# Performance work log

Measured on AMD Instinct MI355X. Metric: run time of the kernel, lower is better.

The kernel has to match this reference:

```python
import jax, jax.numpy as jnp
import numpy as np

EMBED_DIM = 512
NUM_HEADS = 8
HEAD_DIM = EMBED_DIM // NUM_HEADS
REL_MAX = 16
NUM_POS_IDS = 2 * REL_MAX + 1 + 1  # 34 (directed + padding id)
PADDING_IDX = 0
B, S = 2, 2048


def setup_inputs() -> dict:
    key = jax.random.key(0)
    ks = jax.random.split(key, 9)
    Q = jax.random.normal(ks[0], (B, S, EMBED_DIM), dtype=jnp.float32)
    K = jax.random.normal(ks[1], (B, S, EMBED_DIM), dtype=jnp.float32)
    V = jax.random.normal(ks[2], (B, S, EMBED_DIM), dtype=jnp.float32)
    rel_pos_ids = jax.random.randint(ks[3], (B, S, S), 0, NUM_POS_IDS, dtype=jnp.int64) if jax.config.jax_enable_x64 else jax.random.randint(ks[3], (B, S, S), 0, NUM_POS_IDS, dtype=jnp.int32)
    scale = 0.02
    Wq = jax.random.normal(ks[4], (EMBED_DIM, EMBED_DIM), dtype=jnp.float32) * scale
    Wk = jax.random.normal(ks[5], (EMBED_DIM, EMBED_DIM), dtype=jnp.float32) * scale
    Wv = jax.random.normal(ks[6], (EMBED_DIM, EMBED_DIM), dtype=jnp.float32) * scale
    Wo = jax.random.normal(ks[7], (EMBED_DIM, EMBED_DIM), dtype=jnp.float32) * scale
    rel_emb = jax.random.normal(ks[8], (NUM_POS_IDS, EMBED_DIM), dtype=jnp.float32) * scale
    rel_emb = rel_emb.at[PADDING_IDX].set(0.0)  # nn.Embedding padding_idx row is zero
    return {"Q": Q, "K": K, "V": V, "rel_pos_ids": rel_pos_ids,
            "Wq": Wq, "Wk": Wk, "Wv": Wv, "Wo": Wo, "rel_emb": rel_emb}


def _proj(x, W):
    # Linear (no bias) then strided head split: view(B, S, head_dim, H) -> (B, H, S, head_dim)
    b, s, _ = x.shape
    y = x @ W.T
    return y.reshape(b, s, HEAD_DIM, NUM_HEADS).transpose(0, 3, 1, 2)


def _forward(Q, K, V, rel_pos_ids, Wq, Wk, Wv, Wo, rel_emb):
    b, sq, _ = Q.shape
    Qp = _proj(Q, Wq)  # (B, H, Sq, hd)
    Kp = _proj(K, Wk)  # (B, H, Sk, hd)
    Vp = _proj(V, Wv)  # (B, H, Sk, hd)

    # rel_embeds split per head with the same strided layout: (P, hd, H) -> (H, P, hd)
    R = rel_emb.reshape(NUM_POS_IDS, HEAD_DIM, NUM_HEADS).transpose(2, 0, 1)
    # Q_rel: (B, H, Sq, P)
    Q_rel = jnp.einsum('bhsd,hpd->bhsp', Qp, R)
    # gather per-pair relative bias: (B, H, Sq, Sk)
    rel_shift = jnp.take_along_axis(Q_rel, rel_pos_ids[:, None, :, :], axis=3)
    mask = (rel_pos_ids == PADDING_IDX)[:, None, :, :]
    rel_shift = jnp.where(mask, -jnp.inf, rel_shift)

    energy = (jnp.einsum('bhqd,bhkd->bhqk', Qp, Kp) + rel_shift) / jnp.sqrt(jnp.float32(HEAD_DIM))
    attn = jax.nn.softmax(energy, axis=-1)
    out = jnp.einsum('bhqk,bhkd->bhqd', attn, Vp)  # (B, H, Sq, hd)
    # inverse of strided split: (B, Sq, hd, H) -> flatten last two
    out = out.transpose(0, 2, 3, 1).reshape(b, sq, EMBED_DIM)
    return out @ Wo.T


def reference(Q, K, V, rel_pos_ids, Wq, Wk, Wv, Wo, rel_emb):
    return _forward(Q, K, V, rel_pos_ids, Wq, Wk, Wv, Wo, rel_emb)
```

## Files before the change

### kernel.cpp

```cpp
#include <hip/hip_runtime.h>
#include <cstdint>
#include <cstddef>

#define SEQ   2048
#define BBAT  2
#define EMBED 512
#define NH    8
#define HD    64
#define NPOS  34

typedef __bf16 bf16;
typedef __bf16 bf16x8 __attribute__((ext_vector_type(8)));
typedef float  f32x4  __attribute__((ext_vector_type(4)));
typedef int    int32x4 __attribute__((ext_vector_type(4)));

#define ESCALE 0.1803368801111204f

__device__ __forceinline__ f32x4 mfma16(bf16x8 a, bf16x8 b, f32x4 c){
  return __builtin_amdgcn_mfma_f32_16x16x32_bf16(a, b, c, 0, 0, 0);
}

__global__ __launch_bounds__(256) void k_prep(
    const float* __restrict__ Q, const float* __restrict__ K, const float* __restrict__ V,
    const float* __restrict__ Wq, const float* __restrict__ Wk,
    const float* __restrict__ Wv, const float* __restrict__ Wo,
    const float* __restrict__ RE,
    bf16* __restrict__ Qb, bf16* __restrict__ Kb, bf16* __restrict__ Vb,
    bf16* __restrict__ Wall, bf16* __restrict__ Rb)
{
  const int NCONV = 3*524288;
  const int NW = 196608, NO = 262144;
  int i = blockIdx.x*256 + threadIdx.x;
  if (i < NCONV){
    int tsel = i >> 19, j = i & 524287;
    const float* s = tsel==0 ? Q : (tsel==1 ? K : V);
    bf16* d       = tsel==0 ? Qb : (tsel==1 ? Kb : Vb);
    float4 v = ((const float4*)s)[j];
    union { bf16 e[4]; ushort4 u; } pk;
    pk.e[0]=(bf16)v.x; pk.e[1]=(bf16)v.y; pk.e[2]=(bf16)v.z; pk.e[3]=(bf16)v.w;
    ((ushort4*)d)[j] = pk.u;
  } else {
    int j = i - NCONV;
    if (j < NW){
      int w  = j >> 16;
      int r  = j & 65535;
      int np = r >> 7, c4 = (r & 127) << 2;
      const float* W = (w==0) ? Wq : ((w==1) ? Wk : Wv);
      int src = ((np & 63) << 3) + (np >> 6);
      float4 v = *(const float4*)(W + (size_t)src*512 + c4);
      union { bf16 e[4]; ushort4 u; } pk;
      pk.e[0]=(bf16)v.x; pk.e[1]=(bf16)v.y; pk.e[2]=(bf16)v.z; pk.e[3]=(bf16)v.w;
      *(ushort4*)(Wall + (size_t)w*262144 + (size_t)np*512 + c4) = pk.u;
    } else if (j < NW + NO){
      int jj = j - NW;
      int n = jj >> 9, kp = jj & 511;
      int src = ((kp & 63) << 3) + (kp >> 6);
      Wall[(size_t)3*262144 + (size_t)n*512 + kp] = (bf16)Wo[(size_t)n*512 + src];
    } else {
      int jj = j - NW - NO;
      if (jj < 8*48*64){
        int h  = jj / (48*64);
        int r2 = jj - h*(48*64);
        int p  = r2 >> 6, dd = r2 & 63;
        float v = (p < NPOS) ? RE[(size_t)p*512 + dd*8 + h] : 0.f;
        Rb[jj] = (bf16)v;
      }
    }
  }
}

__global__ __launch_bounds__(256,2) void k_gemm_proj(
    const bf16* __restrict__ Qb, const bf16* __restrict__ Kb, const bf16* __restrict__ Vb,
    const bf16* __restrict__ W,  bf16* __restrict__ Qp, bf16* __restrict__ Kp, bf16* __restrict__ Vt)
{
  const bf16* A  = blockIdx.z==0 ? Qb : (blockIdx.z==1 ? Kb : Vb);
  const bf16* Bw = W + (size_t)blockIdx.z*262144;

  __shared__ __align__(16) bf16 As[128][72];
  __shared__ __align__(16) bf16 Bs[64][72];
  const int t = threadIdx.x;
  const int w = t >> 6, lane = t & 63, l15 = lane & 15, quad = lane >> 4;
  const int wm = (w & 1) * 64, wn = (w >> 1) * 32;
  const int m0 = blockIdx.y * 128, n0 = blockIdx.x * 64;

  f32x4 acc[4][2];
  #pragma unroll
  for (int mt=0; mt<4; ++mt)
    #pragma unroll
    for (int nt=0; nt<2; ++nt) acc[mt][nt] = (f32x4){0.f,0.f,0.f,0.f};

  for (int kt = 0; kt < 512; kt += 64){
    #pragma unroll
    for (int i = 0; i < 4; ++i){
      int lin = t + 256*i;
      int r = lin >> 3, c8 = (lin & 7) << 3;
      *(uint4*)&As[r][c8] = *(const uint4*)(A + (size_t)(m0 + r)*512 + kt + c8);
    }
    #pragma unroll
    for (int i = 0; i < 2; ++i){
      int lin = t + 256*i;
      int r = lin >> 3, c8 = (lin & 7) << 3;
      *(uint4*)&Bs[r][c8] = *(const uint4*)(Bw + (size_t)(n0 + r)*512 + kt + c8);
    }
    __syncthreads();
    #pragma unroll
    for (int ks = 0; ks < 2; ++ks){
      bf16x8 am[4], bn[2];
      #pragma unroll
      for (int x=0;x<4;++x) am[x] = *(const bf16x8*)&As[wm + x*16 + l15][ks*32 + quad*8];
      #pragma unroll
      for (int y=0;y<2;++y) bn[y] = *(const bf16x8*)&Bs[wn + y*16 + l15][ks*32 + quad*8];
      #pragma unroll
      for (int mt=0;mt<4;++mt)
        #pragma unroll
        for (int nt=0;nt<2;++nt)
          acc[mt][nt] = mfma16(am[mt], bn[nt], acc[mt][nt]);
    }
    __syncthreads();
  }

  if (blockIdx.z != 2){
    bf16* C = blockIdx.z==0 ? Qp : Kp;
    const float scl = (blockIdx.z==0) ? ESCALE : 1.0f;
    #pragma unroll
    for (int mt=0;mt<4;++mt)
      #pragma unroll
      for (int r=0;r<4;++r){
        int m = m0 + wm + mt*16 + quad*4 + r;
        #pragma unroll
        for (int nt=0;nt<2;++nt)
          C[(size_t)m*512 + n0 + wn + nt*16 + l15] = (bf16)(acc[mt][nt][r] * scl);
      }
  } else {
    bf16 (*VT)[136] = (bf16(*)[136])As;
    #pragma unroll
    for (int mt=0;mt<4;++mt)
      #pragma unroll
      for (int r=0;r<4;++r){
        int m = wm + mt*16 + quad*4 + r;
        #pragma unroll
        for (int nt=0;nt<2;++nt)
          VT[wn + nt*16 + l15][m] = (bf16)acc[mt][nt][r];
      }
    __syncthreads();
    const int h = blockIdx.x, b = m0 >> 11, s0 = m0 & 2047;
    const int n = t >> 2, c0 = (t & 3) * 32;
    bf16* dst = Vt + ((size_t)((b*NH + h)*HD + n))*SEQ + s0 + c0;
    #pragma unroll
    for (int i = 0; i < 4; ++i)
      *(uint4*)(dst + i*8) = *(const uint4*)&VT[n][c0 + i*8];
  }
}

__global__ __launch_bounds__(256,2) void k_gemm_out(
    const bf16* __restrict__ A, const bf16* __restrict__ Bw, float* __restrict__ C)
{
  __shared__ __align__(16) bf16 As[64][72];
  __shared__ __align__(16) bf16 Bs[64][72];
  const int t = threadIdx.x;
  const int w = t >> 6, lane = t & 63, l15 = lane & 15, quad = lane >> 4;
  const int wm = (w & 1) * 32, wn = (w >> 1) * 32;
  const int m0 = blockIdx.y * 64, n0 = blockIdx.x * 64;

  f32x4 acc[2][2];
  #pragma unroll
  for (int mt=0; mt<2; ++mt)
    #pragma unroll
    for (int nt=0; nt<2; ++nt) acc[mt][nt] = (f32x4){0.f,0.f,0.f,0.f};

  for (int kt = 0; kt < 512; kt += 64){
    #pragma unroll
    for (int i = 0; i < 2; ++i){
      int lin = t + 256*i;
      int r = lin >> 3, c8 = (lin & 7) << 3;
      *(uint4*)&As[r][c8] = *(const uint4*)(A  + (size_t)(m0 + r)*512 + kt + c8);
      *(uint4*)&Bs[r][c8] = *(const uint4*)(Bw + (size_t)(n0 + r)*512 + kt + c8);
    }
    __syncthreads();
    #pragma unroll
    for (int ks = 0; ks < 2; ++ks){
      bf16x8 am[2], bn[2];
      #pragma unroll
      for (int x=0;x<2;++x) am[x] = *(const bf16x8*)&As[wm + x*16 + l15][ks*32 + quad*8];
      #pragma unroll
      for (int y=0;y<2;++y) bn[y] = *(const bf16x8*)&Bs[wn + y*16 + l15][ks*32 + quad*8];
      #pragma unroll
      for (int mt=0;mt<2;++mt)
        #pragma unroll
        for (int nt=0;nt<2;++nt)
          acc[mt][nt] = mfma16(am[mt], bn[nt], acc[mt][nt]);
    }
    __syncthreads();
  }
  #pragma unroll
  for (int mt=0;mt<2;++mt)
    #pragma unroll
    for (int r=0;r<4;++r){
      int m = m0 + wm + mt*16 + quad*4 + r;
      #pragma unroll
      for (int nt=0;nt<2;++nt)
        C[(size_t)m*512 + n0 + wn + nt*16 + l15] = acc[mt][nt][r];
    }
}

__global__ __launch_bounds__(256,2) void k_attn(
    const bf16* __restrict__ Qp, const bf16* __restrict__ Kp,
    const bf16* __restrict__ Vt, const bf16* __restrict__ Rb,
    const int* __restrict__ ids, bf16* __restrict__ Out)
{
  __shared__ __align__(16) bf16 Ks[128][72];
  __shared__ __align__(16) bf16 Vs[64][136];
  __shared__ __align__(16) bf16 Ps[64][136];
  __shared__ float lut[64][35];
  __shared__ float lsum_s[128];

  const int t = threadIdx.x;
  const int b = blockIdx.z, h = blockIdx.y;
  const int q0 = blockIdx.x * 64;
  const int w = t >> 6, lane = t & 63, l15 = lane & 15, quad = lane >> 4;
  const int qh = w & 1, kh = w >> 1;

  const size_t idb = (size_t)b*SEQ*SEQ;

  int32x4 nid[2][4];
  #pragma unroll
  for (int mt=0; mt<2; ++mt)
    #pragma unroll
    for (int nt=0; nt<4; ++nt)
      nid[mt][nt] = *(const int32x4*)(ids + idb
          + (size_t)(q0 + qh*32 + mt*16 + l15)*SEQ
          + kh*64 + nt*16 + quad*4);

  {
    const bf16* qbrow = Qp + (size_t)(b*SEQ + q0 + w*16 + l15)*EMBED + h*HD;
    bf16x8 ab0 = *(const bf16x8*)(qbrow + quad*8);
    bf16x8 ab1 = *(const bf16x8*)(qbrow + 32 + quad*8);
    const bf16* rh = Rb + h*3072;
    #pragma unroll
    for (int nt = 0; nt < 3; ++nt){
      bf16x8 r0 = *(const bf16x8*)(rh + (nt*16 + l15)*64 + quad*8);
      bf16x8 r1 = *(const bf16x8*)(rh + (nt*16 + l15)*64 + 32 + quad*8);
      f32x4 c = (f32x4){0.f,0.f,0.f,0.f};
      c = mfma16(ab0, r0, c);
      c = mfma16(ab1, r1, c);
      int p = nt*16 + l15;
      if (p < NPOS){
        #pragma unroll
        for (int r = 0; r < 4; ++r)
          lut[w*16 + quad*4 + r][p] = (p == 0) ? -1e30f : c[r];
      }
    }
  }

  bf16x8 bq[2][2];
  #pragma unroll
  for (int mt = 0; mt < 2; ++mt){
    const bf16* qrow = Qp + (size_t)(b*SEQ + q0 + qh*32 + mt*16 + l15)*EMBED + h*HD;
    bq[mt][0] = *(const bf16x8*)(qrow + quad*8);
    bq[mt][1] = *(const bf16x8*)(qrow + 32 + quad*8);
  }

  const bf16* kbase = Kp + (size_t)b*SEQ*EMBED + h*HD;
  const bf16* vbase = Vt + (size_t)(b*NH + h)*HD*SEQ;

  f32x4 acc[2][2];
  #pragma unroll
  for (int mt=0;mt<2;++mt)
    #pragma unroll
    for (int nt=0;nt<2;++nt) acc[mt][nt] = (f32x4){0.f,0.f,0.f,0.f};
  float lsum[2] = {0.f, 0.f};

  for (int kt = 0; kt < 16; ++kt){
    const int k0 = kt * 128;
    #pragma unroll
    for (int i = 0; i < 4; ++i){
      int lin = t + 256*i;
      int r = lin >> 3, c8 = (lin & 7) << 3;
      *(uint4*)&Ks[r][c8] = *(const uint4*)(kbase + (size_t)(k0 + r)*EMBED + c8);
    }
    #pragma unroll
    for (int i = 0; i < 4; ++i){
      int lin = t + 256*i;
      int d = lin >> 4, c8 = (lin & 15) << 3;
      *(uint4*)&Vs[d][c8] = *(const uint4*)(vbase + (size_t)d*SEQ + k0 + c8);
    }
    __syncthreads();

    float wv[2][4][4];
    #pragma unroll
    for (int mt = 0; mt < 2; ++mt){
      const float* lr = &lut[qh*32 + mt*16 + l15][0];
      #pragma unroll
      for (int nt = 0; nt < 4; ++nt){
        int32x4 v = nid[mt][nt];
        wv[mt][nt][0] = lr[v[0]];
        wv[mt][nt][1] = lr[v[1]];
        wv[mt][nt][2] = lr[v[2]];
        wv[mt][nt][3] = lr[v[3]];
      }
    }

    if (kt < 15){
      #pragma unroll
      for (int mt = 0; mt < 2; ++mt)
        #pragma unroll
        for (int nt = 0; nt < 4; ++nt)
          nid[mt][nt] = *(const int32x4*)(ids + idb
              + (size_t)(q0 + qh*32 + mt*16 + l15)*SEQ
              + (k0 + 128) + kh*64 + nt*16 + quad*4);
    }

    f32x4 sf[2][4];
    __builtin_amdgcn_s_setprio(1);
    #pragma unroll
    for (int nt = 0; nt < 4; ++nt){
      bf16x8 ak0 = *(const bf16x8*)&Ks[kh*64 + nt*16 + l15][quad*8];
      bf16x8 ak1 = *(const bf16x8*)&Ks[kh*64 + nt*16 + l15][32 + quad*8];
      #pragma unroll
      for (int mt = 0; mt < 2; ++mt){
        f32x4 c = (f32x4){0.f,0.f,0.f,0.f};
        c = mfma16(ak0, bq[mt][0], c);
        c = mfma16(ak1, bq[mt][1], c);
        sf[mt][nt] = c;
      }
    }
    __builtin_amdgcn_s_setprio(0);

    #pragma unroll
    for (int mt = 0; mt < 2; ++mt){
      #pragma unroll
      for (int nt = 0; nt < 4; ++nt){
        union { bf16 e[4]; uint2 u; } pk;
        float p0 = __builtin_amdgcn_exp2f(sf[mt][nt][0] + wv[mt][nt][0]);
        float p1 = __builtin_amdgcn_exp2f(sf[mt][nt][1] + wv[mt][nt][1]);
        float p2 = __builtin_amdgcn_exp2f(sf[mt][nt][2] + wv[mt][nt][2]);
        float p3 = __builtin_amdgcn_exp2f(sf[mt][nt][3] + wv[mt][nt][3]);
        pk.e[0] = (bf16)p0; pk.e[1] = (bf16)p1;
        pk.e[2] = (bf16)p2; pk.e[3] = (bf16)p3;
        lsum[mt] += (p0 + p1) + (p2 + p3);
        *(uint2*)&Ps[qh*32 + mt*16 + l15][kh*64 + nt*16 + quad*4] = pk.u;
      }
    }
    __syncthreads();

    __builtin_amdgcn_s_setprio(1);
    #pragma unroll
    for (int kk = 0; kk < 4; ++kk){
      bf16x8 ap[2];
      #pragma unroll
      for (int mt = 0; mt < 2; ++mt)
        ap[mt] = *(const bf16x8*)&Ps[qh*32 + mt*16 + l15][kk*32 + quad*8];
      #pragma unroll
      for (int nt = 0; nt < 2; ++nt){
        bf16x8 bv = *(const bf16x8*)&Vs[kh*32 + nt*16 + l15][kk*32 + quad*8];
        #pragma unroll
        for (int mt = 0; mt < 2; ++mt)
          acc[mt][nt] = mfma16(ap[mt], bv, acc[mt][nt]);
      }
    }
    __builtin_amdgcn_s_setprio(0);
    __syncthreads();
  }

  #pragma unroll
  for (int mt = 0; mt < 2; ++mt){
    float v = lsum[mt];
    v += __shfl_xor(v, 16);
    v += __shfl_xor(v, 32);
    if (quad == 0) lsum_s[kh*64 + qh*32 + mt*16 + l15] = v;
  }
  __syncthreads();

  #pragma unroll
  for (int mt = 0; mt < 2; ++mt){
    #pragma unroll
    for (int r = 0; r < 4; ++r){
      int ql = qh*32 + mt*16 + quad*4 + r;
      float inv = __builtin_amdgcn_rcpf(lsum_s[ql] + lsum_s[64 + ql]);
      #pragma unroll
      for (int nt = 0; nt < 2; ++nt){
        int d = kh*32 + nt*16 + l15;
        Out[(size_t)(b*SEQ + q0 + ql)*EMBED + h*HD + d] = (bf16)(acc[mt][nt][r]*inv);
      }
    }
  }
}

extern "C" void kernel_launch(void* const* d_in, const int* in_sizes, int n_in,
                              void* d_out, int out_size, void* d_ws, size_t ws_size,
                              hipStream_t stream)
{
  (void)in_sizes; (void)n_in; (void)out_size;
  const float* Q  = (const float*)d_in[0];
  const float* K  = (const float*)d_in[1];
  const float* V  = (const float*)d_in[2];
  const int*   ID = (const int*)d_in[3];
  const float* Wq = (const float*)d_in[4];
  const float* Wk = (const float*)d_in[5];
  const float* Wv = (const float*)d_in[6];
  const float* Wo = (const float*)d_in[7];
  const float* RE = (const float*)d_in[8];
  float* out = (float*)d_out;

  const size_t MB = (size_t)1 << 20;
  if (ws_size < 36*MB) return;
  char* ws = (char*)d_ws;
  bf16*  Qb    = (bf16*)(ws + 0*MB);
  bf16*  Kb    = (bf16*)(ws + 4*MB);
  bf16*  Vb    = (bf16*)(ws + 8*MB);
  bf16*  Qp    = (bf16*)(ws + 12*MB);
  bf16*  Kp    = (bf16*)(ws + 16*MB);
  bf16*  Vt    = (bf16*)(ws + 20*MB);
  bf16*  Wall  = (bf16*)(ws + 24*MB);
  bf16*  Wop   = Wall + (size_t)3*262144;
  bf16*  Rb    = (bf16*)(ws + 26*MB);
  bf16*  AO    = (bf16*)(ws + 0*MB);

  k_prep      <<<dim3(8032),    256, 0, stream>>>(Q, K, V, Wq, Wk, Wv, Wo, RE,
                                                  Qb, Kb, Vb, Wall, Rb);
  k_gemm_proj <<<dim3(8,32,3),  256, 0, stream>>>(Qb, Kb, Vb, Wall, Qp, Kp, Vt);
  k_attn      <<<dim3(32,8,2),  256, 0, stream>>>(Qp, Kp, Vt, Rb, ID, AO);
  k_gemm_out  <<<dim3(8,64),    256, 0, stream>>>(AO, Wop, out);
}
```

Measured before the change: 190.6 us.

## Register-prefetch K/V tiles and split PV by key half to drop a barrier

K and V tiles for the next iteration are now loaded from global memory into registers during the current iteration, with the loop unrolled by two to ping-pong the register buffers. The PV product is repartitioned so each wave uses only the probabilities it wrote itself (its key half) across all 64 output columns. This removes the barrier between the softmax write and the PV read. Partial accumulators from the two key halves are combined through shared memory at the end. The LUT is also transposed to lutT[p][q] to change the LDS bank access pattern. The trade is higher register pressure (extra uint4 buffers and doubled accumulators) under launch_bounds(256,2), plus an added cross-wave reduction.

```diff
diff --git a/kernel.cpp b/kernel.cpp
--- a/kernel.cpp
+++ b/kernel.cpp
@@ -18,6 +18,12 @@
 
 __device__ __forceinline__ f32x4 mfma16(bf16x8 a, bf16x8 b, f32x4 c){
   return __builtin_amdgcn_mfma_f32_16x16x32_bf16(a, b, c, 0, 0, 0);
+}
+
+__device__ __forceinline__ void barrier_lgkm(){
+  asm volatile("s_waitcnt lgkmcnt(0)" ::: "memory");
+  __builtin_amdgcn_s_barrier();
+  __builtin_amdgcn_sched_barrier(0);
 }
 
 __global__ __launch_bounds__(256) void k_prep(
@@ -211,7 +217,7 @@
   __shared__ __align__(16) bf16 Ks[128][72];
   __shared__ __align__(16) bf16 Vs[64][136];
   __shared__ __align__(16) bf16 Ps[64][136];
-  __shared__ float lut[64][35];
+  __shared__ float lutT[35][64];
   __shared__ float lsum_s[128];
 
   const int t = threadIdx.x;
@@ -221,6 +227,20 @@
   const int qh = w & 1, kh = w >> 1;
 
   const size_t idb = (size_t)b*SEQ*SEQ;
+  const bf16* kbase = Kp + (size_t)b*SEQ*EMBED + h*HD;
+  const bf16* vbase = Vt + (size_t)(b*NH + h)*HD*SEQ;
+
+  uint4 ka[4], va[4], kb2[4], vb2[4];
+  #pragma unroll
+  for (int i=0;i<4;++i){
+    int lin = t + 256*i; int r = lin>>3, c8 = (lin&7)<<3;
+    ka[i] = *(const uint4*)(kbase + (size_t)r*EMBED + c8);
+  }
+  #pragma unroll
+  for (int i=0;i<4;++i){
+    int lin = t + 256*i; int d = lin>>4, c8 = (lin&15)<<3;
+    va[i] = *(const uint4*)(vbase + (size_t)d*SEQ + c8);
+  }
 
   int32x4 nid[2][4];
   #pragma unroll
@@ -247,7 +267,7 @@
       if (p < NPOS){
         #pragma unroll
         for (int r = 0; r < 4; ++r)
-          lut[w*16 + quad*4 + r][p] = (p == 0) ? -1e30f : c[r];
+          lutT[p][w*16 + quad*4 + r] = (p == 0) ? -1e30f : c[r];
       }
     }
   }
@@ -260,107 +280,116 @@
     bq[mt][1] = *(const bf16x8*)(qrow + 32 + quad*8);
   }
 
-  const bf16* kbase = Kp + (size_t)b*SEQ*EMBED + h*HD;
-  const bf16* vbase = Vt + (size_t)(b*NH + h)*HD*SEQ;
-
-  f32x4 acc[2][2];
+  f32x4 acc[2][4];
   #pragma unroll
   for (int mt=0;mt<2;++mt)
     #pragma unroll
-    for (int nt=0;nt<2;++nt) acc[mt][nt] = (f32x4){0.f,0.f,0.f,0.f};
+    for (int nt=0;nt<4;++nt) acc[mt][nt] = (f32x4){0.f,0.f,0.f,0.f};
   float lsum[2] = {0.f, 0.f};
 
-  for (int kt = 0; kt < 16; ++kt){
-    const int k0 = kt * 128;
-    #pragma unroll
-    for (int i = 0; i < 4; ++i){
-      int lin = t + 256*i;
-      int r = lin >> 3, c8 = (lin & 7) << 3;
-      *(uint4*)&Ks[r][c8] = *(const uint4*)(kbase + (size_t)(k0 + r)*EMBED + c8);
-    }
-    #pragma unroll
-    for (int i = 0; i < 4; ++i){
-      int lin = t + 256*i;
-      int d = lin >> 4, c8 = (lin & 15) << 3;
-      *(uint4*)&Vs[d][c8] = *(const uint4*)(vbase + (size_t)d*SEQ + k0 + c8);
-    }
-    __syncthreads();
-
-    float wv[2][4][4];
-    #pragma unroll
-    for (int mt = 0; mt < 2; ++mt){
-      const float* lr = &lut[qh*32 + mt*16 + l15][0];
-      #pragma unroll
-      for (int nt = 0; nt < 4; ++nt){
-        int32x4 v = nid[mt][nt];
-        wv[mt][nt][0] = lr[v[0]];
-        wv[mt][nt][1] = lr[v[1]];
-        wv[mt][nt][2] = lr[v[2]];
-        wv[mt][nt][3] = lr[v[3]];
-      }
-    }
-
-    if (kt < 15){
-      #pragma unroll
-      for (int mt = 0; mt < 2; ++mt)
-        #pragma unroll
-        for (int nt = 0; nt < 4; ++nt)
-          nid[mt][nt] = *(const int32x4*)(ids + idb
-              + (size_t)(q0 + qh*32 + mt*16 + l15)*SEQ
-              + (k0 + 128) + kh*64 + nt*16 + quad*4);
-    }
-
-    f32x4 sf[2][4];
-    __builtin_amdgcn_s_setprio(1);
-    #pragma unroll
-    for (int nt = 0; nt < 4; ++nt){
-      bf16x8 ak0 = *(const bf16x8*)&Ks[kh*64 + nt*16 + l15][quad*8];
-      bf16x8 ak1 = *(const bf16x8*)&Ks[kh*64 + nt*16 + l15][32 + quad*8];
-      #pragma unroll
-      for (int mt = 0; mt < 2; ++mt){
-        f32x4 c = (f32x4){0.f,0.f,0.f,0.f};
-        c = mfma16(ak0, bq[mt][0], c);
-        c = mfma16(ak1, bq[mt][1], c);
-        sf[mt][nt] = c;
-      }
-    }
-    __builtin_amdgcn_s_setprio(0);
-
-    #pragma unroll
-    for (int mt = 0; mt < 2; ++mt){
-      #pragma unroll
-      for (int nt = 0; nt < 4; ++nt){
-        union { bf16 e[4]; uint2 u; } pk;
-        float p0 = __builtin_amdgcn_exp2f(sf[mt][nt][0] + wv[mt][nt][0]);
-        float p1 = __builtin_amdgcn_exp2f(sf[mt][nt][1] + wv[mt][nt][1]);
-        float p2 = __builtin_amdgcn_exp2f(sf[mt][nt][2] + wv[mt][nt][2]);
-        float p3 = __builtin_amdgcn_exp2f(sf[mt][nt][3] + wv[mt][nt][3]);
-        pk.e[0] = (bf16)p0; pk.e[1] = (bf16)p1;
-        pk.e[2] = (bf16)p2; pk.e[3] = (bf16)p3;
-        lsum[mt] += (p0 + p1) + (p2 + p3);
-        *(uint2*)&Ps[qh*32 + mt*16 + l15][kh*64 + nt*16 + quad*4] = pk.u;
-      }
-    }
-    __syncthreads();
-
-    __builtin_amdgcn_s_setprio(1);
-    #pragma unroll
-    for (int kk = 0; kk < 4; ++kk){
-      bf16x8 ap[2];
-      #pragma unroll
-      for (int mt = 0; mt < 2; ++mt)
-        ap[mt] = *(const bf16x8*)&Ps[qh*32 + mt*16 + l15][kk*32 + quad*8];
-      #pragma unroll
-      for (int nt = 0; nt < 2; ++nt){
-        bf16x8 bv = *(const bf16x8*)&Vs[kh*32 + nt*16 + l15][kk*32 + quad*8];
-        #pragma unroll
-        for (int mt = 0; mt < 2; ++mt)
-          acc[mt][nt] = mfma16(ap[mt], bv, acc[mt][nt]);
-      }
-    }
-    __builtin_amdgcn_s_setprio(0);
-    __syncthreads();
-  }
+#define ATTN_BODY(KT, WK, WV, LK, LV)                                           \
+  {                                                                             \
+    barrier_lgkm();              \
+    _Pragma("unroll")                                                           \
+    for (int i = 0; i < 4; ++i){                                                \
+      int lin = t + 256*i; int r = lin>>3, c8 = (lin&7)<<3;                     \
+      *(uint4*)&Ks[r][c8] = WK[i];                                              \
+    }                                                                           \
+    _Pragma("unroll")                                                           \
+    for (int i = 0; i < 4; ++i){                                                \
+      int lin = t + 256*i; int d = lin>>4, c8 = (lin&15)<<3;                    \
+      *(uint4*)&Vs[d][c8] = WV[i];                                              \
+    }                                                                           \
+    if ((KT) < 15){                                                             \
+      _Pragma("unroll")                                                         \
+      for (int i = 0; i < 4; ++i){                                              \
+        int lin = t + 256*i; int r = lin>>3, c8 = (lin&7)<<3;                   \
+        LK[i] = *(const uint4*)(kbase + (size_t)(((KT)+1)*128 + r)*EMBED + c8); \
+      }                                                                         \
+      _Pragma("unroll")                                                         \
+      for (int i = 0; i < 4; ++i){                                              \
+        int lin = t + 256*i; int d = lin>>4, c8 = (lin&15)<<3;                  \
+        LV[i] = *(const uint4*)(vbase + (size_t)d*SEQ + ((KT)+1)*128 + c8);     \
+      }                                                                         \
+    }                                                                           \
+    barrier_lgkm();                \
+    float wvv[2][4][4];                                                         \
+    _Pragma("unroll")                                                           \
+    for (int mt = 0; mt < 2; ++mt){                                             \
+      const float* lcol = &lutT[0][qh*32 + mt*16 + l15];                        \
+      _Pragma("unroll")                                                         \
+      for (int nt = 0; nt < 4; ++nt){                                           \
+        int32x4 v = nid[mt][nt];                                                \
+        wvv[mt][nt][0] = lcol[v[0] << 6];                                       \
+        wvv[mt][nt][1] = lcol[v[1] << 6];                                       \
+        wvv[mt][nt][2] = lcol[v[2] << 6];                                       \
+        wvv[mt][nt][3] = lcol[v[3] << 6];                                       \
+      }                                                                         \
+    }                                                                           \
+    if ((KT) < 15){                                                             \
+      _Pragma("unroll")                                                         \
+      for (int mt = 0; mt < 2; ++mt)                                            \
+        _Pragma("unroll")                                                       \
+        for (int nt = 0; nt < 4; ++nt)                                          \
+          nid[mt][nt] = *(const int32x4*)(ids + idb                             \
+              + (size_t)(q0 + qh*32 + mt*16 + l15)*SEQ                          \
+              + (((KT)+1)*128) + kh*64 + nt*16 + quad*4);                       \
+    }                                                                           \
+    f32x4 sf[2][4];                                                             \
+    __builtin_amdgcn_s_setprio(1);                                              \
+    _Pragma("unroll")                                                           \
+    for (int nt = 0; nt < 4; ++nt){                                             \
+      bf16x8 ak0 = *(const bf16x8*)&Ks[kh*64 + nt*16 + l15][quad*8];            \
+      bf16x8 ak1 = *(const bf16x8*)&Ks[kh*64 + nt*16 + l15][32 + quad*8];       \
+      _Pragma("unroll")                                                         \
+      for (int mt = 0; mt < 2; ++mt){                                           \
+        f32x4 c = (f32x4){0.f,0.f,0.f,0.f};                                     \
+        c = mfma16(ak0, bq[mt][0], c);                                          \
+        c = mfma16(ak1, bq[mt][1], c);                                          \
+        sf[mt][nt] = c;                                                         \
+      }                                                                         \
+    }                                                                           \
+    __builtin_amdgcn_s_setprio(0);                                              \
+    _Pragma("unroll")                                                           \
+    for (int mt = 0; mt < 2; ++mt){                                             \
+      _Pragma("unroll")                                                         \
+      for (int nt = 0; nt < 4; ++nt){                                           \
+        union { bf16 e[4]; uint2 u; } pk;                                       \
+        float p0 = __builtin_amdgcn_exp2f(sf[mt][nt][0] + wvv[mt][nt][0]);      \
+        float p1 = __builtin_amdgcn_exp2f(sf[mt][nt][1] + wvv[mt][nt][1]);      \
+        float p2 = __builtin_amdgcn_exp2f(sf[mt][nt][2] + wvv[mt][nt][2]);      \
+        float p3 = __builtin_amdgcn_exp2f(sf[mt][nt][3] + wvv[mt][nt][3]);      \
+        pk.e[0] = (bf16)p0; pk.e[1] = (bf16)p1;                                 \
+        pk.e[2] = (bf16)p2; pk.e[3] = (bf16)p3;                                 \
+        lsum[mt] += (p0 + p1) + (p2 + p3);                                      \
+        *(uint2*)&Ps[qh*32 + mt*16 + l15][kh*64 + nt*16 + quad*4] = pk.u;       \
+      }                                                                         \
+    }                                                                           \
+    __builtin_amdgcn_s_setprio(1);                                              \
+    _Pragma("unroll")                                                           \
+    for (int ks = 0; ks < 2; ++ks){                                             \
+      bf16x8 ap[2];                                                             \
+      _Pragma("unroll")                                                         \
+      for (int mt = 0; mt < 2; ++mt)                                            \
+        ap[mt] = *(const bf16x8*)&Ps[qh*32 + mt*16 + l15][kh*64 + ks*32 + quad*8]; \
+      _Pragma("unroll")                                                         \
+      for (int nt = 0; nt < 4; ++nt){                                           \
+        bf16x8 bv = *(const bf16x8*)&Vs[nt*16 + l15][kh*64 + ks*32 + quad*8];   \
+        _Pragma("unroll")                                                       \
+        for (int mt = 0; mt < 2; ++mt)                                          \
+          acc[mt][nt] = mfma16(ap[mt], bv, acc[mt][nt]);                        \
+      }                                                                         \
+    }                                                                           \
+    __builtin_amdgcn_s_setprio(0);                                              \
+  }
+
+  for (int kt2 = 0; kt2 < 16; kt2 += 2){
+    ATTN_BODY(kt2,     ka,  va,  kb2, vb2)
+    ATTN_BODY(kt2 + 1, kb2, vb2, ka,  va)
+  }
+#undef ATTN_BODY
+
+  __syncthreads();
 
   #pragma unroll
   for (int mt = 0; mt < 2; ++mt){
@@ -369,7 +398,30 @@
     v += __shfl_xor(v, 32);
     if (quad == 0) lsum_s[kh*64 + qh*32 + mt*16 + l15] = v;
   }
+
+  float* xch = (float*)&Ps[0][0];
+  {
+    const int oh = 1 - kh;
+    #pragma unroll
+    for (int mt = 0; mt < 2; ++mt)
+      #pragma unroll
+      for (int n2 = 0; n2 < 2; ++n2){
+        f32x4 a = acc[mt][2*oh + n2];
+        #pragma unroll
+        for (int r = 0; r < 4; ++r)
+          xch[(qh*2 + oh)*1024 + (mt*16 + quad*4 + r)*32 + n2*16 + l15] = a[r];
+      }
+  }
   __syncthreads();
+
+  #pragma unroll
+  for (int mt = 0; mt < 2; ++mt)
+    #pragma unroll
+    for (int n2 = 0; n2 < 2; ++n2){
+      #pragma unroll
+      for (int r = 0; r < 4; ++r)
+        acc[mt][2*kh + n2][r] += xch[(qh*2 + kh)*1024 + (mt*16 + quad*4 + r)*32 + n2*16 + l15];
+    }
 
   #pragma unroll
   for (int mt = 0; mt < 2; ++mt){
@@ -378,9 +430,9 @@
       int ql = qh*32 + mt*16 + quad*4 + r;
       float inv = __builtin_amdgcn_rcpf(lsum_s[ql] + lsum_s[64 + ql]);
       #pragma unroll
-      for (int nt = 0; nt < 2; ++nt){
-        int d = kh*32 + nt*16 + l15;
-        Out[(size_t)(b*SEQ + q0 + ql)*EMBED + h*HD + d] = (bf16)(acc[mt][nt][r]*inv);
+      for (int n2 = 0; n2 < 2; ++n2){
+        int d = kh*32 + n2*16 + l15;
+        Out[(size_t)(b*SEQ + q0 + ql)*EMBED + h*HD + d] = (bf16)(acc[mt][2*kh + n2][r]*inv);
       }
     }
   }
```

Result: slower. 295.1 us (+54.8%).
